# Performance work log

Measured on AMD Instinct MI355X. Metric: run time of the kernel, lower is better.

## Reference

```python
import jax, jax.numpy as jnp
import numpy as np

B = 512
ND, ED = 40, 160
N0, C1, C2 = 706, 512, 400
E0 = 8000
DIM_C = 16
BN_EPS = 1e-5


def _np_graphs():
    rng = np.random.default_rng(0)
    off_d = np.arange(B)[:, None] * ND
    dei = np.stack([(rng.integers(0, ND, (B, ED)) + off_d).ravel(),
                    (rng.integers(0, ND, (B, ED)) + off_d).ravel()]).astype(np.int32)
    dbatch = np.repeat(np.arange(B), ND).astype(np.int32)
    off_c = np.arange(B)[:, None] * N0
    ei0 = np.stack([(rng.integers(0, N0, (B, E0)) + off_c).ravel(),
                    (rng.integers(0, N0, (B, E0)) + off_c).ravel()])

    def surj(n, c):
        a = np.concatenate([np.arange(c), rng.integers(0, c, n - c)])
        rng.shuffle(a)
        return a
    c0, c1 = surj(N0, C1), surj(C1, C2)
    cl0 = (c0[None] + np.arange(B)[:, None] * C1).ravel()
    cl1 = (c1[None] + np.arange(B)[:, None] * C2).ravel()
    # pooled edge_index for GAT layer 1 (PyG max_pool: map, drop self loops, coalesce)
    e1 = cl0[ei0]
    e1 = e1[:, e1[0] != e1[1]]
    e1 = np.unique(e1, axis=1)
    return dei, dbatch, ei0.astype(np.int32), e1.astype(np.int32), cl0.astype(np.int32), cl1.astype(np.int32)


def _bn(x, gamma=None, beta=None):
    # training-mode BatchNorm1d forward (biased batch var), affine optional
    mu = x.mean(0)
    var = x.var(0)
    xh = (x - mu) * jax.lax.rsqrt(var + BN_EPS)
    if gamma is None:
        return xh
    return xh * gamma + beta


def _gat(x, ei, W, a_src, a_dst, bias):
    # PyG GATConv, heads=1, self loops added, leaky_relu slope 0.2
    n = x.shape[0]
    loop = jnp.arange(n, dtype=ei.dtype)
    src = jnp.concatenate([ei[0], loop])
    dst = jnp.concatenate([ei[1], loop])
    h = x @ W  # [N, F]
    logit = jax.nn.leaky_relu((h * a_src).sum(-1)[src] + (h * a_dst).sum(-1)[dst], 0.2)
    m = jax.ops.segment_max(logit, dst, num_segments=n)
    e = jnp.exp(logit - m[dst])
    s = jax.ops.segment_sum(e, dst, num_segments=n)
    alpha = e / s[dst]
    return jax.ops.segment_sum(h[src] * alpha[:, None], dst, num_segments=n) + bias


def _forward(drug_x, cell_x, gin0_W1, gin0_b1, gin0_W2, gin0_b2, gin0_g, gin0_be, gin1_W1, gin1_b1, gin1_W2, gin1_b2, gin1_g, gin1_be, gin2_W1, gin2_b1, gin2_W2, gin2_b2, gin2_g, gin2_be, demb_W, demb_b, gat0_W, gat0_as, gat0_ad, gat0_b, gat1_W, gat1_as, gat1_ad, gat1_b, cemb_W1, cemb_b1, cemb_W2, cemb_b2, reg_W1, reg_b1, reg_W2, reg_b2, reg_W3, reg_b3, drug_edge_index, drug_batch, cell_edge_index0, cell_edge_index1, cluster0, cluster1):
    nd = drug_x.shape[0]
    x = drug_x
    reps = []
    gin = ((gin0_W1, gin0_b1, gin0_W2, gin0_b2, gin0_g, gin0_be),
           (gin1_W1, gin1_b1, gin1_W2, gin1_b2, gin1_g, gin1_be),
           (gin2_W1, gin2_b1, gin2_W2, gin2_b2, gin2_g, gin2_be))
    for W1, b1, W2, b2, g, be in gin:
        agg = jax.ops.segment_sum(x[drug_edge_index[0]], drug_edge_index[1], num_segments=nd)
        x = jax.nn.relu(jax.nn.relu((x + agg) @ W1 + b1) @ W2 + b2)
        x = _bn(x, g, be)
        reps.append(x)
    xd = jax.ops.segment_max(jnp.concatenate(reps, -1), drug_batch, num_segments=B)  # [B,384]
    xd = jax.nn.relu(xd @ demb_W + demb_b)  # dropout = identity (eval)
    # cell branch: GAT + relu, cluster max_pool, BN (affine=False), twice
    xc = jax.nn.relu(_gat(cell_x, cell_edge_index0, gat0_W, gat0_as, gat0_ad, gat0_b))
    xc = _bn(jax.ops.segment_max(xc, cluster0, num_segments=B * C1))
    xc = jax.nn.relu(_gat(xc, cell_edge_index1, gat1_W, gat1_as, gat1_ad, gat1_b))
    xc = _bn(jax.ops.segment_max(xc, cluster1, num_segments=B * C2))
    xc = xc.reshape(B, C2 * DIM_C)
    xc = jax.nn.relu(xc @ cemb_W1 + cemb_b1)
    xc = jax.nn.relu(xc @ cemb_W2 + cemb_b2)
    h = jnp.concatenate([xd, xc], -1)  # [B,384]
    h = jax.nn.elu(h @ reg_W1 + reg_b1)
    h = jax.nn.elu(h @ reg_W2 + reg_b2)
    return h @ reg_W3 + reg_b3  # [B,1]


def setup_inputs():
    dei, dbatch, ei0, ei1, cl0, cl1 = _np_graphs()
    keys = iter(jax.random.split(jax.random.key(0), 64))

    def W(*shape):
        return jax.random.normal(next(keys), shape, jnp.float32) / np.float32(np.sqrt(shape[0]))

    def vec(n):
        return jax.random.normal(next(keys), (n,), jnp.float32) * np.float32(0.3)
    z = lambda n: jnp.zeros((n,), jnp.float32)
    inp = {'drug_x': jax.random.normal(next(keys), (B * ND, 77), jnp.float32),
           'cell_x': jax.random.normal(next(keys), (B * N0, 3), jnp.float32)}
    for i, fin in enumerate((77, 128, 128)):
        inp['gin%d_W1' % i] = W(fin, 128); inp['gin%d_b1' % i] = z(128)
        inp['gin%d_W2' % i] = W(128, 128); inp['gin%d_b2' % i] = z(128)
        inp['gin%d_g' % i] = jnp.ones((128,), jnp.float32); inp['gin%d_be' % i] = z(128)
    inp['demb_W'] = W(3 * 128, 128); inp['demb_b'] = z(128)
    for i, fin in enumerate((3, DIM_C)):
        inp['gat%d_W' % i] = W(fin, DIM_C)
        inp['gat%d_as' % i] = vec(DIM_C)
        inp['gat%d_ad' % i] = vec(DIM_C)
        inp['gat%d_b' % i] = z(DIM_C)
    inp['cemb_W1'] = W(C2 * DIM_C, 1024); inp['cemb_b1'] = z(1024)
    inp['cemb_W2'] = W(1024, 256); inp['cemb_b2'] = z(256)
    inp['reg_W1'] = W(384, 384); inp['reg_b1'] = z(384)
    inp['reg_W2'] = W(384, 384); inp['reg_b2'] = z(384)
    inp['reg_W3'] = W(384, 1); inp['reg_b3'] = z(1)
    inp['drug_edge_index'] = jnp.asarray(dei)
    inp['drug_batch'] = jnp.asarray(dbatch)
    inp['cell_edge_index0'] = jnp.asarray(ei0)
    inp['cell_edge_index1'] = jnp.asarray(ei1)
    inp['cluster0'] = jnp.asarray(cl0)
    inp['cluster1'] = jnp.asarray(cl1)
    return inp


def reference(drug_x, cell_x, gin0_W1, gin0_b1, gin0_W2, gin0_b2, gin0_g, gin0_be, gin1_W1, gin1_b1, gin1_W2, gin1_b2, gin1_g, gin1_be, gin2_W1, gin2_b1, gin2_W2, gin2_b2, gin2_g, gin2_be, demb_W, demb_b, gat0_W, gat0_as, gat0_ad, gat0_b, gat1_W, gat1_as, gat1_ad, gat1_b, cemb_W1, cemb_b1, cemb_W2, cemb_b2, reg_W1, reg_b1, reg_W2, reg_b2, reg_W3, reg_b3, drug_edge_index, drug_batch, cell_edge_index0, cell_edge_index1, cluster0, cluster1):
    return _forward(drug_x, cell_x, gin0_W1, gin0_b1, gin0_W2, gin0_b2, gin0_g, gin0_be, gin1_W1, gin1_b1, gin1_W2, gin1_b2, gin1_g, gin1_be, gin2_W1, gin2_b1, gin2_W2, gin2_b2, gin2_g, gin2_be, demb_W, demb_b, gat0_W, gat0_as, gat0_ad, gat0_b, gat1_W, gat1_as, gat1_ad, gat1_b, cemb_W1, cemb_b1, cemb_W2, cemb_b2, reg_W1, reg_b1, reg_W2, reg_b2, reg_W3, reg_b3, drug_edge_index, drug_batch, cell_edge_index0, cell_edge_index1, cluster0, cluster1)
```

## Files before the change

kernel.cpp:

```cpp
#include <hip/hip_runtime.h>
#include <math.h>

typedef __attribute__((ext_vector_type(8))) short bfrag;
typedef __attribute__((ext_vector_type(4))) float ffrag;

__device__ __forceinline__ unsigned short f2b(float v) {
  return (unsigned short)((__float_as_uint(v) + 0x8000u) >> 16);
}
__device__ __forceinline__ float b2f(unsigned short u) {
  return __uint_as_float((unsigned int)u << 16);
}

__global__ __launch_bounds__(256)
void k_w2bt6(const float* __restrict__ w0, const float* __restrict__ w1,
             const float* __restrict__ w2, const float* __restrict__ w3,
             const float* __restrict__ w4, const float* __restrict__ w5,
             unsigned short* __restrict__ out) {
  int t = blockIdx.x*256 + threadIdx.x;
  if (t >= 128*136) return;
  int L = blockIdx.y;
  const float* W; int Ksrc = 128;
  switch (L) {
    case 0: W = w0; Ksrc = 77; break;
    case 1: W = w1; break;
    case 2: W = w2; break;
    case 3: W = w3; break;
    case 4: W = w4; break;
    default: W = w5; break;
  }
  int n = t / 136, k = t - n*136;
  float v = (k < Ksrc) ? W[(size_t)k*128 + n] : 0.f;
  out[(size_t)L*128*136 + t] = f2b(v);
}

template<int KIN, int BNIN>
__global__ __launch_bounds__(256)
void k_gin_agg_b(const float* __restrict__ xg, const float* __restrict__ st,
                 const int* __restrict__ esrc, const int* __restrict__ edst,
                 unsigned short* __restrict__ xin) {
  __shared__ float xb[40*128];
  __shared__ unsigned short scsr[160];
  __shared__ int srow[41];
  const int b = blockIdx.x, tid = threadIdx.x, nbase = b*40;
  if (tid <= 40) srow[tid] = 0;
  __syncthreads();
  int rs = -1, rd = -1;
  if (tid < 160) {
    rs = esrc[b*160+tid] - nbase;
    rd = edst[b*160+tid] - nbase;
    atomicAdd(&srow[rd+1], 1);
  }
  for (int i = tid; i < 40*KIN; i += 256) {
    int n = i/KIN, f = i - n*KIN;
    float v = xg[(size_t)(nbase+n)*KIN + f];
    if (BNIN) v = fmaf(v, st[f], st[KIN+f]);
    xb[n*128 + f] = v;
  }
  __syncthreads();
  if (tid == 0) { int run = 0; for (int i = 1; i <= 40; ++i) { run += srow[i]; srow[i] = run; } }
  __syncthreads();
  if (tid < 160) { int slot = atomicAdd(&srow[rd], 1); scsr[slot] = (unsigned short)rs; }
  __syncthreads();
  for (int i = tid; i < 40*128; i += 256) {
    int n = i >> 7, f = i & 127;
    float a = 0.f;
    if (f < KIN) {
      a = xb[n*128 + f];
      int j0 = n ? srow[n-1] : 0, j1 = srow[n];
      for (int j = j0; j < j1; ++j) a += xb[scsr[j]*128 + f];
    }
    xin[(size_t)nbase*128 + i] = f2b(a);
  }
}

__global__ __launch_bounds__(512)
void k_gin_fmfma(const unsigned short* __restrict__ Ax,
                 const unsigned short* __restrict__ W1t,
                 const unsigned short* __restrict__ W2t,
                 const float* __restrict__ b1, const float* __restrict__ b2,
                 float* __restrict__ outp, float* __restrict__ bnp) {
  __shared__ unsigned short Ab[128*136];
  __shared__ unsigned short W1l[128*136];
  __shared__ unsigned short W2l[128*136];
  __shared__ float cred[8*128], cred2[8*128];
  const int tid = threadIdx.x;
  const int row0 = blockIdx.x << 7;
  for (int i = tid; i < 128*17; i += 512) {
    int r = i / 17, c8 = (i - r*17) << 3;
    uint4 v = make_uint4(0,0,0,0);
    if (c8 < 128) v = *(const uint4*)(Ax + (size_t)(row0 + r)*128 + c8);
    *(uint4*)&Ab[r*136 + c8]  = v;
    *(uint4*)&W1l[r*136 + c8] = *(const uint4*)(W1t + r*136 + c8);
    *(uint4*)&W2l[r*136 + c8] = *(const uint4*)(W2t + r*136 + c8);
  }
  __syncthreads();
  const int wave = tid >> 6, lane = tid & 63;
  const int fr = lane & 15, fk = (lane >> 4) << 3;
  const int wrow = wave << 4;
  const int mrow = (lane >> 4) << 2;
  float b1v[8], b2v[8];
#pragma unroll
  for (int n = 0; n < 8; ++n) { b1v[n] = b1[(n<<4) + fr]; b2v[n] = b2[(n<<4) + fr]; }

  ffrag acc[8];
#pragma unroll
  for (int n = 0; n < 8; ++n) acc[n] = (ffrag){0.f,0.f,0.f,0.f};
#pragma unroll
  for (int s = 0; s < 4; ++s) {
    bfrag af = *(const bfrag*)&Ab[(wrow + fr)*136 + (s<<5) + fk];
#pragma unroll
    for (int n = 0; n < 8; ++n) {
      bfrag bf = *(const bfrag*)&W1l[((n<<4) + fr)*136 + (s<<5) + fk];
      acc[n] = __builtin_amdgcn_mfma_f32_16x16x32_bf16(af, bf, acc[n], 0, 0, 0);
    }
  }
#pragma unroll
  for (int n = 0; n < 8; ++n)
#pragma unroll
    for (int r = 0; r < 4; ++r) {
      float v = fmaxf(acc[n][r] + b1v[n], 0.f);
      Ab[(wrow + mrow + r)*136 + (n<<4) + fr] = f2b(v);
    }
  __syncthreads();

  ffrag acc2[8];
#pragma unroll
  for (int n = 0; n < 8; ++n) acc2[n] = (ffrag){0.f,0.f,0.f,0.f};
#pragma unroll
  for (int s = 0; s < 4; ++s) {
    bfrag af = *(const bfrag*)&Ab[(wrow + fr)*136 + (s<<5) + fk];
#pragma unroll
    for (int n = 0; n < 8; ++n) {
      bfrag bf = *(const bfrag*)&W2l[((n<<4) + fr)*136 + (s<<5) + fk];
      acc2[n] = __builtin_amdgcn_mfma_f32_16x16x32_bf16(af, bf, acc2[n], 0, 0, 0);
    }
  }
#pragma unroll
  for (int n = 0; n < 8; ++n) {
    float s = 0.f, q = 0.f;
#pragma unroll
    for (int r = 0; r < 4; ++r) {
      float v = fmaxf(acc2[n][r] + b2v[n], 0.f);
      outp[(size_t)(row0 + wrow + mrow + r)*128 + (n<<4) + fr] = v;
      s += v; q = fmaf(v, v, q);
    }
    s += __shfl_xor(s, 16); s += __shfl_xor(s, 32);
    q += __shfl_xor(q, 16); q += __shfl_xor(q, 32);
    if (lane < 16) { cred[wave*128 + (n<<4) + fr] = s; cred2[wave*128 + (n<<4) + fr] = q; }
  }
  __syncthreads();
  if (tid < 128) {
    float S = 0.f, Q = 0.f;
#pragma unroll
    for (int w = 0; w < 8; ++w) { S += cred[w*128 + tid]; Q += cred2[w*128 + tid]; }
    bnp[blockIdx.x*256 + tid] = S;
    bnp[blockIdx.x*256 + 128 + tid] = Q;
  }
}

__global__ __launch_bounds__(128)
void k_drug_pool_bn(const float* __restrict__ p0, const float* __restrict__ p1,
                    const float* __restrict__ p2,
                    const float* __restrict__ s0, const float* __restrict__ s1,
                    const float* __restrict__ s2,
                    float* __restrict__ xd) {
  int b = blockIdx.x, f = threadIdx.x;
  const float* ps[3] = {p0,p1,p2};
  const float* ss[3] = {s0,s1,s2};
#pragma unroll
  for (int L = 0; L < 3; ++L) {
    float sc = ss[L][f], sh = ss[L][128+f];
    float m = -3.0e38f;
    const float* p = ps[L] + (size_t)b*40*128 + f;
    for (int n = 0; n < 40; ++n) m = fmaxf(m, fmaf(p[n*128], sc, sh));
    xd[(size_t)b*384 + L*128 + f] = m;
  }
}

template<int ACT, int PART, int BNA, int NPA, int ACTA, int BNP>
__global__ __launch_bounds__(256)
void k_gemm(const float* __restrict__ A, int lda,
            const float* __restrict__ B, int ldb,
            const float* __restrict__ bias,
            float* __restrict__ C, int ldc, int Kchunk,
            long pstrideC, long pstrideA,
            const float* __restrict__ abias,
            const float* __restrict__ bnst,
            float* __restrict__ bnp) {
  __shared__ __align__(16) float As[32][68];
  __shared__ __align__(16) float Bs[32][68];
  const int tid = threadIdx.x;
  const int tx = tid & 15, ty = tid >> 4;
  const int row0 = blockIdx.y << 6, col0 = blockIdx.x << 6;
  const int kb = blockIdx.z * Kchunk;
  if (PART) C += (size_t)blockIdx.z * pstrideC;
  float acc[4][4] = {{0.f}};
  for (int k0 = 0; k0 < Kchunk; k0 += 32) {
#pragma unroll
    for (int i = 0; i < 2; ++i) {
      int idx = tid + (i << 8);
      int r = idx >> 3, c = (idx & 7) << 2;
      const float* ap = A + (size_t)(row0 + r)*lda + (kb + k0 + c);
      float4 v = *(const float4*)ap;
      if (NPA > 1) {
#pragma unroll
        for (int z = 1; z < NPA; ++z) {
          float4 p = *(const float4*)(ap + (size_t)z*pstrideA);
          v.x += p.x; v.y += p.y; v.z += p.z; v.w += p.w;
        }
        const float* ab = abias + (kb + k0 + c);
        v.x += ab[0]; v.y += ab[1]; v.z += ab[2]; v.w += ab[3];
        if (ACTA == 1) {
          v.x=fmaxf(v.x,0.f); v.y=fmaxf(v.y,0.f); v.z=fmaxf(v.z,0.f); v.w=fmaxf(v.w,0.f);
        } else if (ACTA == 2) {
          v.x = v.x>0.f?v.x:expm1f(v.x); v.y = v.y>0.f?v.y:expm1f(v.y);
          v.z = v.z>0.f?v.z:expm1f(v.z); v.w = v.w>0.f?v.w:expm1f(v.w);
        }
      }
      if (BNA) {
        int fb = (kb + k0 + c) & 15;
        float4 sc = *(const float4*)&bnst[fb];
        float4 sh = *(const float4*)&bnst[16 + fb];
        v.x = fmaf(v.x, sc.x, sh.x); v.y = fmaf(v.y, sc.y, sh.y);
        v.z = fmaf(v.z, sc.z, sh.z); v.w = fmaf(v.w, sc.w, sh.w);
      }
      int sw = ((c >> 2) & 7) << 2;
      int rs = r ^ sw;
      As[c+0][rs]=v.x; As[c+1][rs]=v.y; As[c+2][rs]=v.z; As[c+3][rs]=v.w;
    }
#pragma unroll
    for (int i = 0; i < 2; ++i) {
      int idx = tid + (i << 8);
      int r = idx >> 4, c = (idx & 15) << 2;
      *(float4*)&Bs[r][c] = *(const float4*)(B + (size_t)(kb + k0 + r)*ldb + (col0 + c));
    }
    __syncthreads();
#pragma unroll
    for (int kk = 0; kk < 32; ++kk) {
      int sw = ((kk >> 2) & 7) << 2;
      float4 av = *(const float4*)&As[kk][(ty << 2) ^ sw];
      float4 bv = *(const float4*)&Bs[kk][tx << 2];
      acc[0][0]=fmaf(av.x,bv.x,acc[0][0]); acc[0][1]=fmaf(av.x,bv.y,acc[0][1]);
      acc[0][2]=fmaf(av.x,bv.z,acc[0][2]); acc[0][3]=fmaf(av.x,bv.w,acc[0][3]);
      acc[1][0]=fmaf(av.y,bv.x,acc[1][0]); acc[1][1]=fmaf(av.y,bv.y,acc[1][1]);
      acc[1][2]=fmaf(av.y,bv.z,acc[1][2]); acc[1][3]=fmaf(av.y,bv.w,acc[1][3]);
      acc[2][0]=fmaf(av.z,bv.x,acc[2][0]); acc[2][1]=fmaf(av.z,bv.y,acc[2][1]);
      acc[2][2]=fmaf(av.z,bv.z,acc[2][2]); acc[2][3]=fmaf(av.z,bv.w,acc[2][3]);
      acc[3][0]=fmaf(av.w,bv.x,acc[3][0]); acc[3][1]=fmaf(av.w,bv.y,acc[3][1]);
      acc[3][2]=fmaf(av.w,bv.z,acc[3][2]); acc[3][3]=fmaf(av.w,bv.w,acc[3][3]);
    }
    __syncthreads();
  }
#pragma unroll
  for (int i = 0; i < 4; ++i) {
    int r = row0 + (ty<<2) + i, c = col0 + (tx<<2);
    float4 v = make_float4(acc[i][0], acc[i][1], acc[i][2], acc[i][3]);
    if (!PART) {
      if (bias) { v.x += bias[c]; v.y += bias[c+1]; v.z += bias[c+2]; v.w += bias[c+3]; }
      if (ACT == 1) { v.x=fmaxf(v.x,0.f); v.y=fmaxf(v.y,0.f); v.z=fmaxf(v.z,0.f); v.w=fmaxf(v.w,0.f); }
      else if (ACT == 2) {
        v.x = v.x>0.f?v.x:expm1f(v.x); v.y = v.y>0.f?v.y:expm1f(v.y);
        v.z = v.z>0.f?v.z:expm1f(v.z); v.w = v.w>0.f?v.w:expm1f(v.w);
      }
    }
    *(float4*)(C + (size_t)r*ldc + c) = v;
  }
}

template<int ACT>
__global__ void k_reduce(const float* __restrict__ parts, int np, long pstride,
                         const float* __restrict__ bias,
                         float* __restrict__ out, int ldo, int M, int N) {
  int t = blockIdx.x*blockDim.x + threadIdx.x;
  if (t >= M*N) return;
  int r = t / N, c = t - r*N;
  float s = 0.f;
  for (int z = 0; z < np; ++z) s += parts[(size_t)z*pstride + t];
  s += bias[c];
  if (ACT == 1) s = fmaxf(s, 0.f);
  else if (ACT == 2) s = s > 0.f ? s : expm1f(s);
  out[(size_t)r*ldo + c] = s;
}

__global__ __launch_bounds__(256)
void k_w2bt(const float* __restrict__ W, unsigned short* __restrict__ Bt) {
  __shared__ float tile[32][33];
  int bk = blockIdx.x << 5, bn = blockIdx.y << 5;
  int c = threadIdx.x & 31, r8 = threadIdx.x >> 5;
#pragma unroll
  for (int i = 0; i < 4; ++i) {
    int r = r8 + (i << 3);
    tile[r][c] = W[(size_t)(bk + r)*1024 + bn + c];
  }
  __syncthreads();
#pragma unroll
  for (int i = 0; i < 4; ++i) {
    int r = r8 + (i << 3);
    Bt[(size_t)(bn + r)*6400 + bk + c] = f2b(tile[c][r]);
  }
}

__global__ void k_a2bn(const float* __restrict__ x, const float* __restrict__ st,
                       unsigned short* __restrict__ o, int total4) {
  int t = blockIdx.x*blockDim.x + threadIdx.x;
  if (t >= total4) return;
  int fb = (t << 2) & 15;
  float4 v = *(const float4*)(x + ((size_t)t << 2));
  float4 sc = *(const float4*)&st[fb];
  float4 sh = *(const float4*)&st[16 + fb];
  ushort4 r;
  r.x = f2b(fmaf(v.x, sc.x, sh.x));
  r.y = f2b(fmaf(v.y, sc.y, sh.y));
  r.z = f2b(fmaf(v.z, sc.z, sh.z));
  r.w = f2b(fmaf(v.w, sc.w, sh.w));
  *(ushort4*)(o + ((size_t)t << 2)) = r;
}

__global__ __launch_bounds__(256)
void k_mfma128(const unsigned short* __restrict__ A,
               const unsigned short* __restrict__ Bt,
               float* __restrict__ C, int ldc, int K,
               int Kchunk, long pstrideC) {
  __shared__ unsigned short Al[2][128*40];
  __shared__ unsigned short Bl[2][128*40];
  const int tid = threadIdx.x;
  const int row0 = blockIdx.y << 7, col0 = blockIdx.x << 7;
  const int kb = blockIdx.z * Kchunk;
  C += (size_t)blockIdx.z * pstrideC;
  const int wave = tid >> 6, lane = tid & 63;
  const int wr = wave >> 1, wc = wave & 1;
  const int fr = lane & 15, fk = (lane >> 4) << 3;
  const int lr = tid >> 1, lco = (tid & 1) << 4;

  ffrag acc[4][4];
#pragma unroll
  for (int i = 0; i < 4; ++i)
#pragma unroll
    for (int n = 0; n < 4; ++n) acc[i][n] = (ffrag){0.f, 0.f, 0.f, 0.f};

  const unsigned short* ag = A  + (size_t)(row0 + lr)*K + kb + lco;
  const unsigned short* bg = Bt + (size_t)(col0 + lr)*K + kb + lco;

  uint4 ra0 = *(const uint4*)ag, ra1 = *(const uint4*)(ag + 8);
  uint4 rb0 = *(const uint4*)bg, rb1 = *(const uint4*)(bg + 8);
  *(uint4*)&Al[0][lr*40 + lco] = ra0; *(uint4*)&Al[0][lr*40 + lco + 8] = ra1;
  *(uint4*)&Bl[0][lr*40 + lco] = rb0; *(uint4*)&Bl[0][lr*40 + lco + 8] = rb1;
  __syncthreads();

  const int NS = Kchunk >> 5;
  int cur = 0;
  for (int s = 0; s < NS; ++s) {
    if (s + 1 < NS) {
      const unsigned short* an = ag + ((s + 1) << 5);
      const unsigned short* bn = bg + ((s + 1) << 5);
      ra0 = *(const uint4*)an; ra1 = *(const uint4*)(an + 8);
      rb0 = *(const uint4*)bn; rb1 = *(const uint4*)(bn + 8);
    }
    bfrag af[4], bf[4];
#pragma unroll
    for (int i = 0; i < 4; ++i) af[i] = *(const bfrag*)&Al[cur][(wr*64 + i*16 + fr)*40 + fk];
#pragma unroll
    for (int n = 0; n < 4; ++n) bf[n] = *(const bfrag*)&Bl[cur][(wc*64 + n*16 + fr)*40 + fk];
#pragma unroll
    for (int i = 0; i < 4; ++i)
#pragma unroll
      for (int n = 0; n < 4; ++n)
        acc[i][n] = __builtin_amdgcn_mfma_f32_16x16x32_bf16(af[i], bf[n], acc[i][n], 0, 0, 0);
    if (s + 1 < NS) {
      cur ^= 1;
      *(uint4*)&Al[cur][lr*40 + lco] = ra0; *(uint4*)&Al[cur][lr*40 + lco + 8] = ra1;
      *(uint4*)&Bl[cur][lr*40 + lco] = rb0; *(uint4*)&Bl[cur][lr*40 + lco + 8] = rb1;
      __syncthreads();
    }
  }
  const int frow = (lane >> 4) << 2;
#pragma unroll
  for (int i = 0; i < 4; ++i)
#pragma unroll
    for (int n = 0; n < 4; ++n) {
      float* cp = C + (size_t)(row0 + wr*64 + i*16 + frow)*ldc + col0 + wc*64 + n*16 + fr;
#pragma unroll
      for (int r = 0; r < 4; ++r) cp[(size_t)r*ldc] = acc[i][n][r];
    }
}

__global__ __launch_bounds__(256)
void k_bn_stats_p(const float* __restrict__ x, int rows, int C, float* __restrict__ parts) {
  __shared__ float sh[256], sh2[256];
  int tid = threadIdx.x;
  int c = tid % C;
  int rpb = 256 / C;
  int r0 = blockIdx.x*rpb + tid / C;
  int rstep = gridDim.x * rpb;
  float s = 0.f, s2 = 0.f;
  for (int r = r0; r < rows; r += rstep) {
    float v = x[(size_t)r*C + c];
    s += v; s2 = fmaf(v, v, s2);
  }
  sh[tid] = s; sh2[tid] = s2; __syncthreads();
  for (int o = 128; o >= C; o >>= 1) {
    if (tid < o) { sh[tid] += sh[tid+o]; sh2[tid] += sh2[tid+o]; }
    __syncthreads();
  }
  if (tid < C) { parts[blockIdx.x*2*C + tid] = sh[tid]; parts[blockIdx.x*2*C + C + tid] = sh2[tid]; }
}

__global__ void k_bn_fin(const float* __restrict__ parts, int nb, int C, float invn,
                         const float* __restrict__ g, const float* __restrict__ be,
                         float* __restrict__ stats) {
  int f = threadIdx.x;
  if (f >= C) return;
  float s = 0.f, s2 = 0.f;
#pragma unroll 4
  for (int z = 0; z < nb; ++z) { s += parts[z*2*C + f]; s2 += parts[z*2*C + C + f]; }
  float mu = s*invn;
  float var = fmaxf(s2*invn - mu*mu, 0.f);
  float rstd = rsqrtf(var + 1e-5f);
  float sc = g ? g[f]*rstd : rstd;
  stats[f] = sc;
  stats[C+f] = (be ? be[f] : 0.f) - mu*sc;
}

template<int NODES, int NPOOL, int KIN, int MAXE, int SORTED, int BNIN, int NT>
__global__ __launch_bounds__(NT, 8)
void k_gat_lds(const float* __restrict__ x,
               const int* __restrict__ esrc, const int* __restrict__ edst, int Earg,
               const float* __restrict__ W, const float* __restrict__ as_,
               const float* __restrict__ ad_, const float* __restrict__ bias,
               const int* __restrict__ cluster,
               const float* __restrict__ instats,
               float* __restrict__ pooled) {
  constexpr int EIT = (MAXE + NT - 1) / NT;
  __shared__ unsigned short shb[NODES*17];
  __shared__ unsigned int spk[MAXE];
  __shared__ float sss[NODES], ssd[NODES];
  __shared__ int srow[NODES+1];
  __shared__ float sWl[KIN*16 + 16];
  __shared__ float sas[16], sad[16];
  __shared__ int schunk[32];
  __shared__ int sr2[2];
  const int b = blockIdx.x;
  const int tid = threadIdx.x;
  const int nbase = b*NODES;

  if (tid < KIN*16) sWl[tid] = W[tid];
  if (tid >= 64 && tid < 80)  sWl[KIN*16 + tid-64] = bias[tid-64];
  if (tid >= 80 && tid < 96)  sas[tid-80] = as_[tid-80];
  if (tid >= 96 && tid < 112) sad[tid-96] = ad_[tid-96];
  if (SORTED && tid == 0) {
    int a = 0, c = Earg;
    while (a < c) { int m = (a+c) >> 1; if (esrc[m] < nbase) a = m+1; else c = m; }
    sr2[0] = a;
    c = Earg;
    int nend = nbase + NODES;
    while (a < c) { int m = (a+c) >> 1; if (esrc[m] < nend) a = m+1; else c = m; }
    sr2[1] = a;
  }
  for (int i = tid; i <= NODES; i += NT) srow[i] = 0;
  __syncthreads();

  int e0, Eblk;
  if (SORTED) { e0 = sr2[0]; Eblk = sr2[1] - sr2[0]; }
  else        { e0 = b*Earg; Eblk = Earg; }

  int ers[EIT], erd[EIT];
#pragma unroll
  for (int it = 0; it < EIT; ++it) {
    int e = tid + it*NT;
    ers[it] = -1; erd[it] = -1;
    if (e < Eblk) {
      ers[it] = esrc[e0+e] - nbase;
      erd[it] = edst[e0+e] - nbase;
      atomicAdd(&srow[erd[it]+1], 1);
    }
  }
  for (int i = tid; i < NODES*16; i += NT) {
    int n = i >> 4, f = i & 15;
    const float* xp = x + (size_t)(nbase + n)*KIN;
    float xq = (f < KIN) ? xp[f] : 0.f;
    if (BNIN && f < KIN) xq = fmaf(xq, instats[f], instats[16+f]);
    float hv = 0.f;
#pragma unroll
    for (int j = 0; j < KIN; ++j) hv = fmaf(__shfl(xq, j, 16), sWl[j*16 + f], hv);
    shb[n*17 + f] = f2b(hv);
    float s1 = hv * sas[f], s2 = hv * sad[f];
#pragma unroll
    for (int m = 8; m >= 1; m >>= 1) { s1 += __shfl_xor(s1, m); s2 += __shfl_xor(s2, m); }
    if (f == 0) { sss[n] = s1; ssd[n] = s2; }
  }
  __syncthreads();

  constexpr int NC = 32, CS = (NODES + NC - 1) / NC;
  if (tid < NC) {
    int run = 0, lo = tid*CS, hi = (tid+1)*CS < NODES ? (tid+1)*CS : NODES;
    for (int i = lo; i < hi; ++i) { run += srow[i+1]; srow[i+1] = run; }
    schunk[tid] = run;
  }
  __syncthreads();
  if (tid == 0) { int base = 0; for (int c = 0; c < NC; ++c) { int t2 = schunk[c]; schunk[c] = base; base += t2; } }
  __syncthreads();
  for (int i = tid; i < NODES; i += NT) srow[i+1] += schunk[i/CS];
  __syncthreads();

#pragma unroll
  for (int it = 0; it < EIT; ++it) {
    if (erd[it] >= 0) {
      int slot = atomicAdd(&srow[erd[it]], 1);
      float l = sss[ers[it]] + ssd[erd[it]];
      l = fmaxf(l, 0.2f*l);
      float ex = __expf(l);
      spk[slot] = ((__float_as_uint(ex) + 0x8000u) & 0xffff0000u) | (unsigned int)ers[it];
    }
  }
  __syncthreads();

  {
    const int lane = tid & 15, grp = tid >> 4;
    for (int n = grp; n < NODES; n += (NT >> 4)) {
      float ls = sss[n] + ssd[n];
      ls = fmaxf(ls, 0.2f*ls);
      float exs = __expf(ls);
      float hn = b2f(shb[n*17 + lane]);
      float accv = exs * hn, sum = exs;
      int j = (n > 0) ? srow[n-1] : 0, j1 = srow[n];
      for (; j + 4 <= j1; j += 4) {
        unsigned int p0 = spk[j], p1 = spk[j+1], p2 = spk[j+2], p3 = spk[j+3];
        float e0 = __uint_as_float(p0 & 0xffff0000u);
        float e1 = __uint_as_float(p1 & 0xffff0000u);
        float e2 = __uint_as_float(p2 & 0xffff0000u);
        float e3 = __uint_as_float(p3 & 0xffff0000u);
        float h0 = b2f(shb[(p0 & 0xffffu)*17 + lane]);
        float h1 = b2f(shb[(p1 & 0xffffu)*17 + lane]);
        float h2 = b2f(shb[(p2 & 0xffffu)*17 + lane]);
        float h3 = b2f(shb[(p3 & 0xffffu)*17 + lane]);
        accv = fmaf(e0, h0, accv); sum += e0;
        accv = fmaf(e1, h1, accv); sum += e1;
        accv = fmaf(e2, h2, accv); sum += e2;
        accv = fmaf(e3, h3, accv); sum += e3;
      }
      for (; j < j1; ++j) {
        unsigned int p0 = spk[j];
        float e0 = __uint_as_float(p0 & 0xffff0000u);
        float h0 = b2f(shb[(p0 & 0xffffu)*17 + lane]);
        accv = fmaf(e0, h0, accv); sum += e0;
      }
      float v = fmaf(accv, 1.f/sum, sWl[KIN*16 + lane]);
      v = fmaxf(v, 0.f);
      atomicMax((int*)pooled + (size_t)cluster[nbase + n]*16 + lane, __float_as_int(v));
    }
  }
}

__global__ __launch_bounds__(64)
void k_gemv_out(const float* __restrict__ parts, long pstrideA,
                const float* __restrict__ abias,
                const float* __restrict__ w,
                const float* __restrict__ b, float* __restrict__ out) {
  int r = blockIdx.x, l = threadIdx.x;
  float s = 0.f;
  for (int k = l; k < 384; k += 64) {
    const float* p = parts + (size_t)r*384 + k;
    float h = p[0] + p[pstrideA] + p[2*pstrideA] + p[3*pstrideA] + abias[k];
    h = h > 0.f ? h : expm1f(h);
    s = fmaf(h, w[k], s);
  }
#pragma unroll
  for (int o = 32; o > 0; o >>= 1) s += __shfl_down(s, o);
  if (l == 0) out[r] = s + b[0];
}

extern "C" void kernel_launch(void* const* d_in, const int* in_sizes, int n_in,
                              void* d_out, int out_size, void* d_ws, size_t ws_size,
                              hipStream_t stream) {
  (void)n_in; (void)out_size;
  const int B = 512;
  const int nd  = B*40;
  const int nc1 = B*512;
  const int nc2 = B*400;
  const int Ec0 = in_sizes[42]/2;
  const int Ec1 = in_sizes[43]/2;

  const float* drug_x = (const float*)d_in[0];
  const float* cell_x = (const float*)d_in[1];
  const float* gW1[3] = {(const float*)d_in[2],(const float*)d_in[8],(const float*)d_in[14]};
  const float* gb1[3] = {(const float*)d_in[3],(const float*)d_in[9],(const float*)d_in[15]};
  const float* gW2[3] = {(const float*)d_in[4],(const float*)d_in[10],(const float*)d_in[16]};
  const float* gb2[3] = {(const float*)d_in[5],(const float*)d_in[11],(const float*)d_in[17]};
  const float* gg [3] = {(const float*)d_in[6],(const float*)d_in[12],(const float*)d_in[18]};
  const float* gbe[3] = {(const float*)d_in[7],(const float*)d_in[13],(const float*)d_in[19]};
  const float* demb_W = (const float*)d_in[20]; const float* demb_b = (const float*)d_in[21];
  const float* gatW[2]  = {(const float*)d_in[22],(const float*)d_in[26]};
  const float* gatAS[2] = {(const float*)d_in[23],(const float*)d_in[27]};
  const float* gatAD[2] = {(const float*)d_in[24],(const float*)d_in[28]};
  const float* gatB[2]  = {(const float*)d_in[25],(const float*)d_in[29]};
  const float* cembW1 = (const float*)d_in[30]; const float* cembb1 = (const float*)d_in[31];
  const float* cembW2 = (const float*)d_in[32]; const float* cembb2 = (const float*)d_in[33];
  const float* regW1 = (const float*)d_in[34]; const float* regb1 = (const float*)d_in[35];
  const float* regW2 = (const float*)d_in[36]; const float* regb2 = (const float*)d_in[37];
  const float* regW3 = (const float*)d_in[38]; const float* regb3 = (const float*)d_in[39];
  const int* dei = (const int*)d_in[40];
  const int* ei0 = (const int*)d_in[42];
  const int* ei1 = (const int*)d_in[43];
  const int* cl0 = (const int*)d_in[44];
  const int* cl1 = (const int*)d_in[45];
  const int Ed  = in_sizes[40]/2;
  const int *dsrc = dei, *ddst = dei + Ed;
  const int *src0 = ei0, *dst0 = ei0 + Ec0;
  const int *src1 = ei1, *dst1 = ei1 + Ec1;
  float* out = (float*)d_out;

  char* base = (char*)d_ws; size_t off = 0;
  auto AL = [&](size_t bytes)->char* { char* p = base + off; off = (off + bytes + 255) & ~(size_t)255; return p; };
  float* h_cat   = (float*)AL((size_t)512*384*4);
  float* xd      = (float*)AL((size_t)512*384*4);
  float* pooled1 = (float*)AL((size_t)nc1*16*4);
  float* pooled2 = (float*)AL((size_t)nc2*16*4);
  float* st_g0   = (float*)AL(256*4);
  float* st_g1   = (float*)AL(256*4);
  float* st_g2   = (float*)AL(256*4);
  float* st16_0  = (float*)AL(32*4);
  float* st16_1  = (float*)AL(32*4);
  float* bparts  = (float*)AL((size_t)320*256*4);
  unsigned short* Wt6 = (unsigned short*)AL((size_t)6*128*136*2);
  char*  S       = base + off;
  if (ws_size < off + (size_t)53*1024*1024) return;

  dim3 b256(256);

  float* pre0 = (float*)(S);
  float* pre1 = pre0 + (size_t)nd*128;
  float* pre2 = pre1 + (size_t)nd*128;
  unsigned short* xin_b = (unsigned short*)(pre2 + (size_t)nd*128);
  float* pre[3] = {pre0, pre1, pre2};
  float* stg[3] = {st_g0, st_g1, st_g2};

  size_t so = 0;
  auto SB = [&](size_t bytes)->char* { char* p = S + so; so = (so + bytes + 255) & ~(size_t)255; return p; };
  unsigned short* Abf = (unsigned short*)SB((size_t)512*6400*2);
  unsigned short* Btb = (unsigned short*)SB((size_t)1024*6400*2);
  float* parts1 = (float*)SB((size_t)8*512*1024*4);
  float* parts2 = (float*)SB((size_t)8*512*256*4);
  float* partsA = (float*)SB((size_t)4*512*384*4);
  float* partsB = (float*)SB((size_t)4*512*384*4);
  float* cembh = (float*)Abf;

  k_w2bt6<<<dim3(68, 6), b256, 0, stream>>>(gW1[0], gW1[1], gW1[2],
                                            gW2[0], gW2[1], gW2[2], Wt6);
  for (int L = 0; L < 3; ++L) {
    if (L == 0)
      k_gin_agg_b<77,0><<<dim3(512), b256, 0, stream>>>(drug_x, nullptr, dsrc, ddst, xin_b);
    else
      k_gin_agg_b<128,1><<<dim3(512), b256, 0, stream>>>(pre[L-1], stg[L-1], dsrc, ddst, xin_b);
    k_gin_fmfma<<<dim3(160), dim3(512), 0, stream>>>(
        xin_b, Wt6 + (size_t)L*128*136, Wt6 + (size_t)(3+L)*128*136,
        gb1[L], gb2[L], pre[L], bparts);
    k_bn_fin<<<dim3(1), dim3(128), 0, stream>>>(bparts, 160, 128, 1.f/nd, gg[L], gbe[L], stg[L]);
  }
  k_drug_pool_bn<<<dim3(512), dim3(128), 0, stream>>>(pre0, pre1, pre2, st_g0, st_g1, st_g2, xd);
  k_gemm<1,0,0,0,0,0><<<dim3(2,8,1), b256, 0, stream>>>(
      xd, 384, demb_W, 128, demb_b, h_cat, 384, 384, 0, 0, nullptr, nullptr, nullptr);

  k_w2bt<<<dim3(200, 32), b256, 0, stream>>>(cembW1, Btb);

  k_gat_lds<706,512,3,8000,0,0,1024><<<dim3(512), dim3(1024), 0, stream>>>(
      cell_x, src0, dst0, Ec0/512, gatW[0], gatAS[0], gatAD[0], gatB[0], cl0,
      nullptr, pooled1);
  k_bn_stats_p<<<dim3(64), b256, 0, stream>>>(pooled1, nc1, 16, bparts);
  k_bn_fin<<<dim3(1), dim3(16), 0, stream>>>(bparts, 64, 16, 1.f/nc1, nullptr, nullptr, st16_0);

  k_gat_lds<512,400,16,8000,1,1,1024><<<dim3(512), dim3(1024), 0, stream>>>(
      pooled1, src1, dst1, Ec1, gatW[1], gatAS[1], gatAD[1], gatB[1], cl1,
      st16_0, pooled2);
  k_bn_stats_p<<<dim3(64), b256, 0, stream>>>(pooled2, nc2, 16, bparts);
  k_bn_fin<<<dim3(1), dim3(16), 0, stream>>>(bparts, 64, 16, 1.f/nc2, nullptr, nullptr, st16_1);

  k_a2bn<<<dim3(3200), b256, 0, stream>>>(pooled2, st16_1, Abf, 512*6400/4);
  k_mfma128<<<dim3(8, 4, 8), b256, 0, stream>>>(
      Abf, Btb, parts1, 1024, 6400, 800, (long)512*1024);
  k_reduce<1><<<dim3((512*1024+255)/256), b256, 0, stream>>>(
      parts1, 8, (long)512*1024, cembb1, cembh, 1024, 512, 1024);
  k_gemm<0,1,0,0,0,0><<<dim3(4,8,8), b256, 0, stream>>>(
      cembh, 1024, cembW2, 256, nullptr, parts2, 256, 128,
      (long)512*256, 0, nullptr, nullptr, nullptr);
  k_reduce<1><<<dim3((512*256+255)/256), b256, 0, stream>>>(
      parts2, 8, (long)512*256, cembb2, h_cat + 128, 384, 512, 256);

  k_gemm<0,1,0,0,0,0><<<dim3(6,8,4), b256, 0, stream>>>(
      h_cat, 384, regW1, 384, nullptr, partsA, 384, 96,
      (long)512*384, 0, nullptr, nullptr, nullptr);
  k_gemm<0,1,0,4,2,0><<<dim3(6,8,4), b256, 0, stream>>>(
      partsA, 384, regW2, 384, nullptr, partsB, 384, 96,
      (long)512*384, (long)512*384, regb1, nullptr, nullptr);
  k_gemv_out<<<dim3(512), dim3(64), 0, stream>>>(
      partsB, (long)512*384, regb2, regW3, regb3, out);
}
```

Measured before the change: 466.4 us.

## Fuse pooled BN stats into GAT kernel and pack bf16 pairs in LDS

Removes the separate BN-statistics kernels after each GAT layer by having each GAT block sum and square-sum its own pooled clusters after aggregation. This relies on each block owning a disjoint slice of pooled rows. The finalizer now reads 512 partials instead of 64. The aggregation also stores h as packed bf16 pairs, so each of 8 lanes per node handles two features, halving LDS gather loads per edge. The trade-off is a longer serial reduction in bn_fin and extra syncs at the tail of the GAT kernel.

Measured after the change: 429.1 us, median of 2. -8.0%, faster.

```diff
diff --git a/kernel.cpp b/kernel.cpp
--- a/kernel.cpp
+++ b/kernel.cpp
@@ -384,27 +384,6 @@
     }
 }
 
-__global__ __launch_bounds__(256)
-void k_bn_stats_p(const float* __restrict__ x, int rows, int C, float* __restrict__ parts) {
-  __shared__ float sh[256], sh2[256];
-  int tid = threadIdx.x;
-  int c = tid % C;
-  int rpb = 256 / C;
-  int r0 = blockIdx.x*rpb + tid / C;
-  int rstep = gridDim.x * rpb;
-  float s = 0.f, s2 = 0.f;
-  for (int r = r0; r < rows; r += rstep) {
-    float v = x[(size_t)r*C + c];
-    s += v; s2 = fmaf(v, v, s2);
-  }
-  sh[tid] = s; sh2[tid] = s2; __syncthreads();
-  for (int o = 128; o >= C; o >>= 1) {
-    if (tid < o) { sh[tid] += sh[tid+o]; sh2[tid] += sh2[tid+o]; }
-    __syncthreads();
-  }
-  if (tid < C) { parts[blockIdx.x*2*C + tid] = sh[tid]; parts[blockIdx.x*2*C + C + tid] = sh2[tid]; }
-}
-
 __global__ void k_bn_fin(const float* __restrict__ parts, int nb, int C, float invn,
                          const float* __restrict__ g, const float* __restrict__ be,
                          float* __restrict__ stats) {
@@ -429,9 +408,9 @@
                const float* __restrict__ ad_, const float* __restrict__ bias,
                const int* __restrict__ cluster,
                const float* __restrict__ instats,
-               float* __restrict__ pooled) {
+               float* __restrict__ pooled, float* __restrict__ bnp) {
   constexpr int EIT = (MAXE + NT - 1) / NT;
-  __shared__ unsigned short shb[NODES*17];
+  __shared__ unsigned int shp[NODES*9];
   __shared__ unsigned int spk[MAXE];
   __shared__ float sss[NODES], ssd[NODES];
   __shared__ int srow[NODES+1];
@@ -482,7 +461,9 @@
     float hv = 0.f;
 #pragma unroll
     for (int j = 0; j < KIN; ++j) hv = fmaf(__shfl(xq, j, 16), sWl[j*16 + f], hv);
-    shb[n*17 + f] = f2b(hv);
+    unsigned int hb = (unsigned int)f2b(hv);
+    unsigned int partner = (unsigned int)__shfl_xor((int)hb, 1);
+    if ((f & 1) == 0) shp[n*9 + (f >> 1)] = hb | (partner << 16);
     float s1 = hv * sas[f], s2 = hv * sad[f];
 #pragma unroll
     for (int m = 8; m >= 1; m >>= 1) { s1 += __shfl_xor(s1, m); s2 += __shfl_xor(s2, m); }
@@ -515,13 +496,15 @@
   __syncthreads();
 
   {
-    const int lane = tid & 15, grp = tid >> 4;
-    for (int n = grp; n < NODES; n += (NT >> 4)) {
+    const int lane = tid & 7, grp = tid >> 3;
+    for (int n = grp; n < NODES; n += (NT >> 3)) {
       float ls = sss[n] + ssd[n];
       ls = fmaxf(ls, 0.2f*ls);
       float exs = __expf(ls);
-      float hn = b2f(shb[n*17 + lane]);
-      float accv = exs * hn, sum = exs;
+      unsigned int hp = shp[n*9 + lane];
+      float aLo = exs * b2f((unsigned short)hp);
+      float aHi = exs * b2f((unsigned short)(hp >> 16));
+      float sum = exs;
       int j = (n > 0) ? srow[n-1] : 0, j1 = srow[n];
       for (; j + 4 <= j1; j += 4) {
         unsigned int p0 = spk[j], p1 = spk[j+1], p2 = spk[j+2], p3 = spk[j+3];
@@ -529,25 +512,52 @@
         float e1 = __uint_as_float(p1 & 0xffff0000u);
         float e2 = __uint_as_float(p2 & 0xffff0000u);
         float e3 = __uint_as_float(p3 & 0xffff0000u);
-        float h0 = b2f(shb[(p0 & 0xffffu)*17 + lane]);
-        float h1 = b2f(shb[(p1 & 0xffffu)*17 + lane]);
-        float h2 = b2f(shb[(p2 & 0xffffu)*17 + lane]);
-        float h3 = b2f(shb[(p3 & 0xffffu)*17 + lane]);
-        accv = fmaf(e0, h0, accv); sum += e0;
-        accv = fmaf(e1, h1, accv); sum += e1;
-        accv = fmaf(e2, h2, accv); sum += e2;
-        accv = fmaf(e3, h3, accv); sum += e3;
+        unsigned int h0 = shp[(p0 & 0xffffu)*9 + lane];
+        unsigned int h1 = shp[(p1 & 0xffffu)*9 + lane];
+        unsigned int h2 = shp[(p2 & 0xffffu)*9 + lane];
+        unsigned int h3 = shp[(p3 & 0xffffu)*9 + lane];
+        aLo = fmaf(e0, b2f((unsigned short)h0), aLo);
+        aHi = fmaf(e0, b2f((unsigned short)(h0 >> 16)), aHi); sum += e0;
+        aLo = fmaf(e1, b2f((unsigned short)h1), aLo);
+        aHi = fmaf(e1, b2f((unsigned short)(h1 >> 16)), aHi); sum += e1;
+        aLo = fmaf(e2, b2f((unsigned short)h2), aLo);
+        aHi = fmaf(e2, b2f((unsigned short)(h2 >> 16)), aHi); sum += e2;
+        aLo = fmaf(e3, b2f((unsigned short)h3), aLo);
+        aHi = fmaf(e3, b2f((unsigned short)(h3 >> 16)), aHi); sum += e3;
       }
       for (; j < j1; ++j) {
         unsigned int p0 = spk[j];
         float e0 = __uint_as_float(p0 & 0xffff0000u);
-        float h0 = b2f(shb[(p0 & 0xffffu)*17 + lane]);
-        accv = fmaf(e0, h0, accv); sum += e0;
+        unsigned int h0 = shp[(p0 & 0xffffu)*9 + lane];
+        aLo = fmaf(e0, b2f((unsigned short)h0), aLo);
+        aHi = fmaf(e0, b2f((unsigned short)(h0 >> 16)), aHi); sum += e0;
       }
-      float v = fmaf(accv, 1.f/sum, sWl[KIN*16 + lane]);
-      v = fmaxf(v, 0.f);
-      atomicMax((int*)pooled + (size_t)cluster[nbase + n]*16 + lane, __float_as_int(v));
-    }
+      float inv = 1.f / sum;
+      float vLo = fmaxf(fmaf(aLo, inv, sWl[KIN*16 + 2*lane]), 0.f);
+      float vHi = fmaxf(fmaf(aHi, inv, sWl[KIN*16 + 2*lane + 1]), 0.f);
+      int* pp = (int*)pooled + (size_t)cluster[nbase + n]*16 + 2*lane;
+      atomicMax(pp,     __float_as_int(vLo));
+      atomicMax(pp + 1, __float_as_int(vHi));
+    }
+  }
+  __syncthreads();
+
+  {
+    float s = 0.f, q = 0.f;
+    const float* po = pooled + (size_t)b*NPOOL*16;
+    int f = tid & 15;
+    for (int r = tid >> 4; r < NPOOL; r += (NT >> 4)) {
+      float v = po[r*16 + f];
+      s += v; q = fmaf(v, v, q);
+    }
+    float* red = (float*)shp;
+    red[tid] = s; red[NT + tid] = q;
+    __syncthreads();
+    for (int o = NT >> 1; o >= 16; o >>= 1) {
+      if (tid < o) { red[tid] += red[tid + o]; red[NT + tid] += red[NT + tid + o]; }
+      __syncthreads();
+    }
+    if (tid < 16) { bnp[b*32 + tid] = red[tid]; bnp[b*32 + 16 + tid] = red[NT + tid]; }
   }
 }
 
@@ -620,7 +630,7 @@
   float* st_g2   = (float*)AL(256*4);
   float* st16_0  = (float*)AL(32*4);
   float* st16_1  = (float*)AL(32*4);
-  float* bparts  = (float*)AL((size_t)320*256*4);
+  float* bparts  = (float*)AL((size_t)512*256*4);
   unsigned short* Wt6 = (unsigned short*)AL((size_t)6*128*136*2);
   char*  S       = base + off;
   if (ws_size < off + (size_t)53*1024*1024) return;
@@ -664,15 +674,13 @@
 
   k_gat_lds<706,512,3,8000,0,0,1024><<<dim3(512), dim3(1024), 0, stream>>>(
       cell_x, src0, dst0, Ec0/512, gatW[0], gatAS[0], gatAD[0], gatB[0], cl0,
-      nullptr, pooled1);
-  k_bn_stats_p<<<dim3(64), b256, 0, stream>>>(pooled1, nc1, 16, bparts);
-  k_bn_fin<<<dim3(1), dim3(16), 0, stream>>>(bparts, 64, 16, 1.f/nc1, nullptr, nullptr, st16_0);
+      nullptr, pooled1, bparts);
+  k_bn_fin<<<dim3(1), dim3(16), 0, stream>>>(bparts, 512, 16, 1.f/nc1, nullptr, nullptr, st16_0);
 
   k_gat_lds<512,400,16,8000,1,1,1024><<<dim3(512), dim3(1024), 0, stream>>>(
       pooled1, src1, dst1, Ec1, gatW[1], gatAS[1], gatAD[1], gatB[1], cl1,
-      st16_0, pooled2);
-  k_bn_stats_p<<<dim3(64), b256, 0, stream>>>(pooled2, nc2, 16, bparts);
-  k_bn_fin<<<dim3(1), dim3(16), 0, stream>>>(bparts, 64, 16, 1.f/nc2, nullptr, nullptr, st16_1);
+      st16_0, pooled2, bparts);
+  k_bn_fin<<<dim3(1), dim3(16), 0, stream>>>(bparts, 512, 16, 1.f/nc2, nullptr, nullptr, st16_1);
 
   k_a2bn<<<dim3(3200), b256, 0, stream>>>(pooled2, st16_1, Abf, 512*6400/4);
   k_mfma128<<<dim3(8, 4, 8), b256, 0, stream>>>(
```
